# Optimization experiments

Measured on AMD Instinct MI355X. Metric: run time of the kernel, lower is better.

Reference implementation:

```python
import jax, jax.numpy as jnp
import numpy as np

B, C_IN, H, W = 4, 128, 32, 128   # W must equal out_channels (fc_out acts on last dim)
C_OUT, NUM_HEADS = 128, 2
BN_EPS = 1e-5


def setup_inputs() -> dict:
    key = jax.random.key(0)
    ks = jax.random.split(key, 14)
    s = 0.05  # small init scale for weights
    d = {
        "x": jax.random.normal(ks[0], (B, C_IN, H, W), jnp.float32),
        "wq": jax.random.normal(ks[1], (C_OUT, C_IN), jnp.float32) * s,
        "bq": jax.random.normal(ks[2], (C_OUT,), jnp.float32) * s,
        "wk": jax.random.normal(ks[3], (C_OUT, C_IN), jnp.float32) * s,
        "bk": jax.random.normal(ks[4], (C_OUT,), jnp.float32) * s,
        "wv": jax.random.normal(ks[5], (C_OUT, C_IN), jnp.float32) * s,
        "bv": jax.random.normal(ks[6], (C_OUT,), jnp.float32) * s,
        "fc_w": jax.random.normal(ks[7], (C_OUT, C_OUT), jnp.float32) * s,
        "fc_b": jax.random.normal(ks[8], (C_OUT,), jnp.float32) * s,
        "bn_gamma": jnp.ones((C_OUT,), jnp.float32),
        "bn_beta": jnp.zeros((C_OUT,), jnp.float32),
        "bn_mean": jax.random.normal(ks[9], (C_OUT,), jnp.float32) * 0.1,
        "bn_var": jax.random.uniform(ks[10], (C_OUT,), jnp.float32, 0.5, 1.5),
        "prelu_a": jnp.full((1,), 0.25, jnp.float32),
    }
    return d


def reference(x, wq, bq, wk, bk, wv, bv, fc_w, fc_b,
              bn_gamma, bn_beta, bn_mean, bn_var, prelu_a):
    b, c_in, h, w = x.shape
    c_out = wq.shape[0]
    nh = NUM_HEADS
    dk = c_out // nh
    L = h * w
    xf = x.reshape(b, c_in, L)                                # (B, Cin, L)
    # 1x1 convs == per-token linear projections
    q = jnp.einsum('oi,bil->bol', wq, xf) + bq[:, None]       # (B, Cout, L)
    k = jnp.einsum('oi,bil->bol', wk, xf) + bk[:, None]
    v = jnp.einsum('oi,bil->bol', wv, xf) + bv[:, None]
    Q = q.reshape(b, nh, dk, L)                               # (B, h, d_k, L)
    K = k.reshape(b, nh, dk, L)
    V = v.reshape(b, nh, dk, L)
    # scaled dot-product attention over the L = H*W tokens
    scores = jnp.einsum('bhdl,bhdm->bhlm', Q, K) / jnp.sqrt(jnp.float32(dk))
    attn = jax.nn.softmax(scores, axis=-1)                    # (B, h, L, L)
    out = jnp.einsum('bhlm,bhdm->bhdl', attn, V)              # (B, h, d_k, L)
    out = out.reshape(b, c_out, h, w)                         # (B, Cout, H, W)
    # fc_out: torch Linear on the LAST dim (W == Cout)
    y = jnp.einsum('bchw,ow->bcho', out, fc_w) + fc_b         # (B, Cout, H, W)
    # BatchNorm2d (eval mode: running stats) over channel dim
    inv = jax.lax.rsqrt(bn_var + BN_EPS)
    y = (y - bn_mean[None, :, None, None]) * (inv * bn_gamma)[None, :, None, None] \
        + bn_beta[None, :, None, None]
    # PReLU (single shared slope); dropout is identity in eval
    y = jnp.where(y > 0, y, prelu_a[0] * y)
    return y
```

## Files before the change

kernel.cpp:

```cpp
#include <hip/hip_runtime.h>

typedef _Float16 f16x8 __attribute__((ext_vector_type(8)));
typedef _Float16 f16x4t __attribute__((ext_vector_type(4)));
typedef __fp16 h16x2 __attribute__((ext_vector_type(2)));
typedef float f32x4 __attribute__((ext_vector_type(4)));
typedef float f32x16 __attribute__((ext_vector_type(16)));
typedef unsigned int uint2v __attribute__((ext_vector_type(2)));

#define L_SZ 4096

__device__ __forceinline__ unsigned short f2h(float f) {
    _Float16 h = (_Float16)f;
    return __builtin_bit_cast(unsigned short, h);
}
__device__ __forceinline__ unsigned int pk2(float a, float b) {
    h16x2 p = __builtin_amdgcn_cvt_pkrtz(a, b);
    return __builtin_bit_cast(unsigned int, p);
}
__device__ __forceinline__ float fexp2(float x) {
#if __has_builtin(__builtin_amdgcn_exp2f)
    return __builtin_amdgcn_exp2f(x);
#else
    return exp2f(x);
#endif
}
__device__ __forceinline__ float frcp(float x) {
#if __has_builtin(__builtin_amdgcn_rcpf)
    return __builtin_amdgcn_rcpf(x);
#else
    return 1.0f / x;
#endif
}
__device__ __forceinline__ void async16(unsigned short* lds, const unsigned short* g) {
    __builtin_amdgcn_global_load_lds(
        (const __attribute__((address_space(1))) unsigned int*)g,
        (__attribute__((address_space(3))) unsigned int*)lds, 16, 0, 0);
}

#define SLOT(row, ci) ((((ci) * 64) + ((row) & 32) + (((row) & 31) ^ (ci))) * 8)

__global__ __launch_bounds__(256) void prep_kernel(
    const float* __restrict__ wq, const float* __restrict__ wk,
    const float* __restrict__ wv, const float* __restrict__ fcw,
    unsigned short* __restrict__ Wimg, unsigned short* __restrict__ Fimg)
{
    int e2 = blockIdx.x * 256 + threadIdx.x;
    if (e2 < 24576) {
        const float* src = (e2 < 8192) ? wq : (e2 < 16384 ? wk : wv);
        float2 v = *(const float2*)&src[(e2 * 2) & 16383];
        int e = e2 * 2;
        int o = e >> 7, ci = (e & 127) >> 3, j = e & 7;
        *(unsigned int*)&Wimg[o * 128 + ((ci ^ (o & 15)) * 8) + j] = pk2(v.x, v.y);
    } else {
        int fe = (e2 - 24576) * 2;
        float2 v = *(const float2*)&fcw[fe];
        int o = fe >> 7, ci = (fe & 127) >> 3, j = fe & 7;
        *(unsigned int*)&Fimg[o * 128 + ((ci ^ (o & 15)) * 8) + j] = pk2(v.x, v.y);
    }
}

__global__ __launch_bounds__(256, 3) void qkv_kernel(
    const float* __restrict__ x,
    const unsigned short* __restrict__ Wimg,
    const float* __restrict__ bq, const float* __restrict__ bk,
    const float* __restrict__ bv,
    unsigned short* __restrict__ Qp, unsigned short* __restrict__ Kp,
    unsigned short* __restrict__ Vp)
{
    int raw = blockIdx.x;
    int v = (raw & 7) * 96 + (raw >> 3);
    int tile = v / 3;
    int p = v - tile * 3;
    int bidx = tile >> 6;
    int l0 = (tile & 63) * 64;
    int tid = threadIdx.x;
    int wave = tid >> 6, lane = tid & 63;
    int c = lane & 15, qd = lane >> 4;

    __shared__ __align__(16) unsigned short Ws[128 * 128];
    __shared__ __align__(16) unsigned short Sc[9216];

    const unsigned short* wsrc = Wimg + p * 16384;
    #pragma unroll
    for (int t = 0; t < 8; ++t)
        async16(&Ws[(t * 256 + wave * 64) * 8], &wsrc[(size_t)(t * 256 + wave * 64 + lane) * 8]);

    unsigned short* Xs = Sc;
    #pragma unroll
    for (int it = 0; it < 8; ++it) {
        int i  = (tid >> 4) + 16 * it;
        int l4 = (tid & 15) * 4;
        const float4 vx = *(const float4*)&x[(bidx * 128 + i) * L_SZ + l0 + l4];
        float vv[4] = {vx.x, vx.y, vx.z, vx.w};
        int ci = i >> 3;
        #pragma unroll
        for (int u = 0; u < 4; ++u) {
            int l = l4 + u;
            Xs[l * 128 + ((ci ^ (l & 15)) * 8) + (i & 7)] = f2h(vv[u]);
        }
    }
    __syncthreads();

    f16x8 afrag[4];
    #pragma unroll
    for (int kc = 0; kc < 4; ++kc) {
        int l = wave * 16 + c;
        int ci = kc * 4 + qd;
        afrag[kc] = *(const f16x8*)&Xs[l * 128 + ((ci ^ (l & 15)) * 8)];
    }
    __syncthreads();

    f32x4 acc[8];
    #pragma unroll
    for (int nt = 0; nt < 8; ++nt) acc[nt] = (f32x4){0.f, 0.f, 0.f, 0.f};

    #pragma unroll
    for (int kc = 0; kc < 4; ++kc) {
        #pragma unroll
        for (int nt = 0; nt < 8; ++nt) {
            int o = nt * 16 + c;
            f16x8 bfrag = *(const f16x8*)&Ws[o * 128 + (((kc * 4 + qd) ^ c) * 8)];
            acc[nt] = __builtin_amdgcn_mfma_f32_16x16x32_f16(afrag[kc], bfrag, acc[nt], 0, 0, 0);
        }
    }

    const float s_q = 0.18033688011f;
    if (p < 2) {
        const float* bias = (p == 0) ? bq : bk;
        unsigned short* Ot = Sc;
        #pragma unroll
        for (int nt = 0; nt < 8; ++nt) {
            int o = nt * 16 + c;
            float bo = bias[o];
            #pragma unroll
            for (int r = 0; r < 4; ++r) {
                int ll = wave * 16 + qd * 4 + r;
                float val = acc[nt][r] + bo;
                if (p == 0) val *= s_q;
                Ot[ll * 144 + o] = f2h(val);
            }
        }
        __syncthreads();
        unsigned short* dst = (p == 0) ? Qp : Kp;
        #pragma unroll
        for (int t = 0; t < 4; ++t) {
            int u = tid + t * 256;
            int row = u >> 4, col = (u & 15) * 8;
            int h = col >> 6, d = col & 63;
            uint4 a = *(const uint4*)&Ot[row * 144 + col];
            *(uint4*)&dst[((size_t)(bidx * 2 + h) * L_SZ + l0 + row) * 64 + d] = a;
        }
    } else {
        unsigned short* Vt = Sc;
        #pragma unroll
        for (int nt = 0; nt < 8; ++nt) {
            int o = nt * 16 + c;
            #pragma unroll
            for (int r = 0; r < 4; ++r) {
                int ll = wave * 16 + qd * 4 + r;
                Vt[o * 72 + ll] = f2h(acc[nt][r] + bv[o]);
            }
        }
        __syncthreads();
        #pragma unroll
        for (int t = 0; t < 2; ++t) {
            int u = tid + t * 256;
            int row = u >> 2;
            int lc = (u & 3) * 16;
            uint4 a0 = *(const uint4*)&Vt[row * 72 + lc];
            uint4 a1 = *(const uint4*)&Vt[row * 72 + lc + 8];
            *(uint4*)&Vp[(size_t)(bidx * 128 + row) * L_SZ + l0 + lc] = a0;
            *(uint4*)&Vp[(size_t)(bidx * 128 + row) * L_SZ + l0 + lc + 8] = a1;
        }
    }
}

__global__ __launch_bounds__(256, 4) void attn_kernel(
    const unsigned short* __restrict__ Qp, const unsigned short* __restrict__ Kp,
    const unsigned short* __restrict__ Vp,
    unsigned short* __restrict__ Opart, float* __restrict__ Mpart, float* __restrict__ Lpart)
{
    int raw = blockIdx.x;
    int blk = (raw & 7) * 128 + (raw >> 3);
    int lt = blk & 31;
    int bh = (blk >> 5) & 7;
    int sp = blk >> 8;
    int l0 = lt * 128;
    int tid = threadIdx.x;
    int wave = tid >> 6, lane = tid & 63;
    int ln = lane & 31, hi = lane >> 5;
    int b = bh >> 1, h = bh & 1;

    __shared__ __align__(16) unsigned short Ks[2][4096];
    __shared__ __align__(16) unsigned short Vs[2][4096];

    const unsigned short* Qb = Qp + (size_t)bh * L_SZ * 64;
    const unsigned short* Kb = Kp + (size_t)bh * L_SZ * 64;
    const unsigned short* Vb = Vp + ((size_t)b * 128 + h * 64) * L_SZ;

    int lq = l0 + wave * 32 + ln;
    f16x8 qf[4];
    #pragma unroll
    for (int kc = 0; kc < 4; ++kc)
        qf[kc] = *(const f16x8*)&Qb[(size_t)lq * 64 + kc * 16 + hi * 8];

    float m_st = 0.f, lsum = 0.f;
    f32x16 acc0 = {}, acc1 = {};

    int mglob = sp * 1024;
    int ci0 = wave, ci1 = 4 + wave;
    int r0_ = (lane & 32) | ((lane & 31) ^ ci0);
    int r1_ = (lane & 32) | ((lane & 31) ^ ci1);

#define STAGE(t, buf) do {                                                        \
        int m0_ = mglob + (t) * 64;                                               \
        async16(&Ks[buf][(wave * 64) * 8],       &Kb[(size_t)(m0_ + r0_) * 64 + ci0 * 8]); \
        async16(&Ks[buf][(256 + wave * 64) * 8], &Kb[(size_t)(m0_ + r1_) * 64 + ci1 * 8]); \
        async16(&Vs[buf][(wave * 64) * 8],       &Vb[(size_t)r0_ * L_SZ + m0_ + ci0 * 8]); \
        async16(&Vs[buf][(256 + wave * 64) * 8], &Vb[(size_t)r1_ * L_SZ + m0_ + ci1 * 8]); \
    } while (0)

#define QK_COMPUTE(kb) do {                                                       \
        s0 = (f32x16){}; s1 = (f32x16){};                                         \
        _Pragma("unroll")                                                         \
        for (int kc = 0; kc < 4; ++kc) {                                          \
            int cd = kc * 2 + hi;                                                 \
            f16x8 k0 = *(const f16x8*)&Ks[kb][SLOT(ln, cd)];                      \
            f16x8 k1 = *(const f16x8*)&Ks[kb][SLOT(32 + ln, cd)];                 \
            s0 = __builtin_amdgcn_mfma_f32_32x32x16_f16(k0, qf[kc], s0, 0, 0, 0); \
            s1 = __builtin_amdgcn_mfma_f32_32x32x16_f16(k1, qf[kc], s1, 0, 0, 0); \
        }                                                                         \
    } while (0)

#define SM_PV_GROUP(kc, vb, e0,e1,e2,e3,e4,e5,e6,e7, rs) do {                     \
        float p0 = fexp2((e0) - m_st); float p1 = fexp2((e1) - m_st);             \
        float p2 = fexp2((e2) - m_st); float p3 = fexp2((e3) - m_st);             \
        float p4 = fexp2((e4) - m_st); float p5 = fexp2((e5) - m_st);             \
        float p6 = fexp2((e6) - m_st); float p7 = fexp2((e7) - m_st);             \
        rs += ((p0 + p1) + (p2 + p3)) + ((p4 + p5) + (p6 + p7));                  \
        unsigned int a0 = pk2(p0, p1), a1 = pk2(p2, p3);                          \
        unsigned int a2 = pk2(p4, p5), a3 = pk2(p6, p7);                          \
        uint2v r02 = __builtin_amdgcn_permlane32_swap(a0, a2, false, false);      \
        uint2v r13 = __builtin_amdgcn_permlane32_swap(a1, a3, false, false);      \
        uint4 pw; pw.x = r02[0]; pw.y = r13[0]; pw.z = r02[1]; pw.w = r13[1];     \
        f16x8 pf = __builtin_bit_cast(f16x8, pw);                                 \
        int cd = (kc) * 2 + hi;                                                   \
        f16x8 v0 = *(const f16x8*)&Vs[vb][SLOT(ln, cd)];                          \
        f16x8 v1 = *(const f16x8*)&Vs[vb][SLOT(32 + ln, cd)];                     \
        acc0 = __builtin_amdgcn_mfma_f32_32x32x16_f16(v0, pf, acc0, 0, 0, 0);     \
        acc1 = __builtin_amdgcn_mfma_f32_32x32x16_f16(v1, pf, acc1, 0, 0, 0);     \
    } while (0)

#define SM_PV_ALL(vb, rsA, rsB) do {                                              \
        SM_PV_GROUP(0, vb, s0[0],s0[1],s0[2],s0[3],s0[4],s0[5],s0[6],s0[7], rsA); \
        SM_PV_GROUP(1, vb, s0[8],s0[9],s0[10],s0[11],s0[12],s0[13],s0[14],s0[15], rsB); \
        SM_PV_GROUP(2, vb, s1[0],s1[1],s1[2],s1[3],s1[4],s1[5],s1[6],s1[7], rsA); \
        SM_PV_GROUP(3, vb, s1[8],s1[9],s1[10],s1[11],s1[12],s1[13],s1[14],s1[15], rsB); \
    } while (0)

    f32x16 s0, s1;

    STAGE(0, 0);
    __syncthreads();
    STAGE(1, 1);
    __builtin_amdgcn_s_setprio(1);
    QK_COMPUTE(0);
    {
        float t_[8];
        #pragma unroll
        for (int r = 0; r < 8; ++r)
            t_[r] = fmaxf(fmaxf(s0[r], s0[r + 8]), s1[r]);
        #pragma unroll
        for (int r = 0; r < 4; ++r)
            t_[r] = fmaxf(fmaxf(t_[r], t_[r + 4]), s1[8 + r]);
        float m01 = fmaxf(fmaxf(t_[0], t_[1]), s1[12]);
        float m23 = fmaxf(fmaxf(t_[2], t_[3]), s1[13]);
        float mx = fmaxf(fmaxf(m01, m23), fmaxf(s1[14], s1[15]));
        m_st = fmaxf(mx, __shfl_xor(mx, 32));
    }
    {
        float rsA = 0.f, rsB = 0.f;
        SM_PV_ALL(0, rsA, rsB);
        lsum = rsA + rsB;
    }
    __builtin_amdgcn_s_setprio(0);

    for (int t = 1; t < 16; ++t) {
        int cur = t & 1;
        __syncthreads();
        if (t < 15) STAGE(t + 1, cur ^ 1);

        __builtin_amdgcn_s_setprio(1);
        QK_COMPUTE(cur);
        float rsA = 0.f, rsB = 0.f;
        SM_PV_ALL(cur, rsA, rsB);
        lsum += rsA + rsB;
        __builtin_amdgcn_s_setprio(0);
    }
#undef STAGE
#undef QK_COMPUTE
#undef SM_PV_GROUP
#undef SM_PV_ALL

    float l_tot = lsum + __shfl_xor(lsum, 32);
    unsigned short* Ow = Opart + (size_t)(sp * 8 + bh) * 64 * 4096;
    #pragma unroll
    for (int r = 0; r < 16; ++r) {
        int d0 = (r & 3) + 8 * (r >> 2) + 4 * hi;
        Ow[(size_t)d0 * 4096 + lq] = f2h(acc0[r]);
        Ow[(size_t)(32 + d0) * 4096 + lq] = f2h(acc1[r]);
    }
    if (hi == 0) {
        Mpart[(sp * 8 + bh) * 4096 + lq] = m_st;
        Lpart[(sp * 8 + bh) * 4096 + lq] = l_tot;
    }
}

__global__ __launch_bounds__(256) void scl_kernel(
    const float* __restrict__ Mp, const float* __restrict__ Lp,
    unsigned short* __restrict__ SclImg)
{
    int gid = blockIdx.x * 256 + threadIdx.x;
    int bh = gid >> 12, l = gid & 4095;
    float m0 = Mp[(0 * 8 + bh) * 4096 + l], m1 = Mp[(1 * 8 + bh) * 4096 + l];
    float m2 = Mp[(2 * 8 + bh) * 4096 + l], m3 = Mp[(3 * 8 + bh) * 4096 + l];
    float mx = fmaxf(fmaxf(m0, m1), fmaxf(m2, m3));
    float a0 = fexp2(m0 - mx), a1 = fexp2(m1 - mx);
    float a2 = fexp2(m2 - mx), a3 = fexp2(m3 - mx);
    float den = a0 * Lp[(0 * 8 + bh) * 4096 + l] + a1 * Lp[(1 * 8 + bh) * 4096 + l]
              + a2 * Lp[(2 * 8 + bh) * 4096 + l] + a3 * Lp[(3 * 8 + bh) * 4096 + l];
    float inv = frcp(den);
    int hl = l >> 7, ww = l & 127;
    int slot = hl * 128 + ((ww + hl) & 127);
    uint2 sc;
    sc.x = pk2(a0 * inv, a1 * inv);
    sc.y = pk2(a2 * inv, a3 * inv);
    *(uint2*)&SclImg[((size_t)bh * 4096 + slot) * 4] = sc;
}

__global__ __launch_bounds__(256, 2) void fc_kernel(
    const unsigned short* __restrict__ Opart,
    const unsigned short* __restrict__ SclImg,
    const unsigned short* __restrict__ Fimg,
    const float* __restrict__ fc_b, const float* __restrict__ bn_g,
    const float* __restrict__ bn_b, const float* __restrict__ bn_m,
    const float* __restrict__ bn_v, const float* __restrict__ prelu_a,
    float* __restrict__ out)
{
    int raw = blockIdx.x;
    int blk = (raw & 7) * 64 + (raw >> 3);
    int r0 = blk * 32;
    int tid = threadIdx.x;
    int c0 = blk & 127;
    int bh = blk >> 6;
    int d = c0 & 63;

    int wave = tid >> 6, lane = tid & 63;
    int c = lane & 15, qd = lane >> 4;
    int rw = r0 + (wave >> 1) * 16;
    int o0 = (wave & 1) * 64;
    int hh = (rw + c) & 31;

    __shared__ __align__(16) unsigned short Fw[128 * 128];
    __shared__ __align__(16) unsigned short SclU[4096 * 4];

    #pragma unroll
    for (int t = 0; t < 8; ++t)
        async16(&SclU[(t * 256 + wave * 64) * 8],
                &SclImg[(size_t)bh * 16384 + (size_t)(t * 256 + wave * 64 + lane) * 8]);
    #pragma unroll
    for (int t = 0; t < 8; ++t)
        async16(&Fw[(t * 256 + wave * 64) * 8],
                &Fimg[(size_t)(t * 256 + wave * 64 + lane) * 8]);

    uint4 ovr[4][4];
    #pragma unroll
    for (int kc = 0; kc < 4; ++kc) {
        int w0 = kc * 32 + qd * 8;
        #pragma unroll
        for (int s = 0; s < 4; ++s)
            ovr[kc][s] = *(const uint4*)&Opart[(size_t)(s * 8 + bh) * 262144 + (size_t)d * 4096 + hh * 128 + w0];
    }
    __syncthreads();

    f16x8 af[4];
    #pragma unroll
    for (int kc = 0; kc < 4; ++kc) {
        int w0 = kc * 32 + qd * 8;
        f16x8 ov0 = __builtin_bit_cast(f16x8, ovr[kc][0]);
        f16x8 ov1 = __builtin_bit_cast(f16x8, ovr[kc][1]);
        f16x8 ov2 = __builtin_bit_cast(f16x8, ovr[kc][2]);
        f16x8 ov3 = __builtin_bit_cast(f16x8, ovr[kc][3]);
        #pragma unroll
        for (int j = 0; j < 8; ++j) {
            int slot = hh * 128 + ((w0 + j + hh) & 127);
            f16x4t sc = *(const f16x4t*)&SclU[slot * 4];
            float v = (float)ov0[j] * (float)sc[0] + (float)ov1[j] * (float)sc[1]
                    + (float)ov2[j] * (float)sc[2] + (float)ov3[j] * (float)sc[3];
            af[kc][j] = (_Float16)v;
        }
    }

    f32x4 acc[4];
    #pragma unroll
    for (int nt = 0; nt < 4; ++nt) acc[nt] = (f32x4){0.f, 0.f, 0.f, 0.f};
    #pragma unroll
    for (int kc = 0; kc < 4; ++kc) {
        #pragma unroll
        for (int nt = 0; nt < 4; ++nt) {
            int o = o0 + nt * 16 + c;
            f16x8 bf = *(const f16x8*)&Fw[o * 128 + (((kc * 4 + qd) ^ c) * 8)];
            acc[nt] = __builtin_amdgcn_mfma_f32_16x16x32_f16(af[kc], bf, acc[nt], 0, 0, 0);
        }
    }

    float pa = prelu_a[0];
    float g  = bn_g[c0] * rsqrtf(bn_v[c0] + 1e-5f);
    float mn = bn_m[c0], bt = bn_b[c0];
    #pragma unroll
    for (int r = 0; r < 4; ++r) {
        int orow = rw + qd * 4 + r;
        #pragma unroll
        for (int nt = 0; nt < 4; ++nt) {
            int o = o0 + nt * 16 + c;
            float y = (acc[nt][r] + fc_b[o] - mn) * g + bt;
            y = y > 0.f ? y : pa * y;
            out[(size_t)orow * 128 + o] = y;
        }
    }
}

extern "C" void kernel_launch(void* const* d_in, const int* in_sizes, int n_in,
                              void* d_out, int out_size, void* d_ws, size_t ws_size,
                              hipStream_t stream) {
    const float* x     = (const float*)d_in[0];
    const float* wq    = (const float*)d_in[1];
    const float* bq    = (const float*)d_in[2];
    const float* wk    = (const float*)d_in[3];
    const float* bk    = (const float*)d_in[4];
    const float* wv    = (const float*)d_in[5];
    const float* bv    = (const float*)d_in[6];
    const float* fcw_f = (const float*)d_in[7];
    const float* fcb   = (const float*)d_in[8];
    const float* bn_g  = (const float*)d_in[9];
    const float* bn_b  = (const float*)d_in[10];
    const float* bn_m  = (const float*)d_in[11];
    const float* bn_v  = (const float*)d_in[12];
    const float* pa    = (const float*)d_in[13];
    float* out = (float*)d_out;

    unsigned short* Qp  = (unsigned short*)d_ws;
    unsigned short* Kp  = Qp + 8 * L_SZ * 64;
    unsigned short* Vp  = Kp + 8 * L_SZ * 64;
    unsigned short* Opart = Vp + 8 * L_SZ * 64;
    float* Mpart = (float*)(Opart + 4 * 8 * 64 * L_SZ);
    float* Lpart = Mpart + 4 * 8 * L_SZ;
    unsigned short* Wimg   = (unsigned short*)(Lpart + 4 * 8 * L_SZ);
    unsigned short* Fimg   = Wimg + 384 * 128;
    unsigned short* SclImg = Fimg + 128 * 128;

    hipLaunchKernelGGL(prep_kernel, dim3(128),  dim3(256), 0, stream,
                       wq, wk, wv, fcw_f, Wimg, Fimg);
    hipLaunchKernelGGL(qkv_kernel,  dim3(768),  dim3(256), 0, stream,
                       x, Wimg, bq, bk, bv, Qp, Kp, Vp);
    hipLaunchKernelGGL(attn_kernel, dim3(1024), dim3(256), 0, stream,
                       Qp, Kp, Vp, Opart, Mpart, Lpart);
    hipLaunchKernelGGL(scl_kernel,  dim3(128),  dim3(256), 0, stream,
                       Mpart, Lpart, SclImg);
    hipLaunchKernelGGL(fc_kernel,   dim3(512),  dim3(256), 0, stream,
                       Opart, SclImg, Fimg, fcb, bn_g, bn_b, bn_m, bn_v, pa, out);
}
```

Before: 157.7 us.

## Double attention block size to 512 threads with 128-key stages

```diff
diff --git a/kernel.cpp b/kernel.cpp
--- a/kernel.cpp
+++ b/kernel.cpp
@@ -175,24 +175,24 @@
     }
 }
 
-__global__ __launch_bounds__(256, 4) void attn_kernel(
+__global__ __launch_bounds__(512, 4) void attn_kernel(
     const unsigned short* __restrict__ Qp, const unsigned short* __restrict__ Kp,
     const unsigned short* __restrict__ Vp,
     unsigned short* __restrict__ Opart, float* __restrict__ Mpart, float* __restrict__ Lpart)
 {
     int raw = blockIdx.x;
-    int blk = (raw & 7) * 128 + (raw >> 3);
-    int lt = blk & 31;
-    int bh = (blk >> 5) & 7;
-    int sp = blk >> 8;
-    int l0 = lt * 128;
+    int blk = (raw & 7) * 64 + (raw >> 3);
+    int lt = blk & 15;
+    int bh = (blk >> 4) & 7;
+    int sp = blk >> 7;
+    int l0 = lt * 256;
     int tid = threadIdx.x;
     int wave = tid >> 6, lane = tid & 63;
     int ln = lane & 31, hi = lane >> 5;
     int b = bh >> 1, h = bh & 1;
 
-    __shared__ __align__(16) unsigned short Ks[2][4096];
-    __shared__ __align__(16) unsigned short Vs[2][4096];
+    __shared__ __align__(16) unsigned short Ks[2][8192];
+    __shared__ __align__(16) unsigned short Vs[2][8192];
 
     const unsigned short* Qb = Qp + (size_t)bh * L_SZ * 64;
     const unsigned short* Kb = Kp + (size_t)bh * L_SZ * 64;
@@ -208,31 +208,35 @@
     f32x16 acc0 = {}, acc1 = {};
 
     int mglob = sp * 1024;
-    int ci0 = wave, ci1 = 4 + wave;
+    int wv = wave & 3, sh = wave >> 2;
+    int ci0 = wv, ci1 = 4 + wv;
     int r0_ = (lane & 32) | ((lane & 31) ^ ci0);
     int r1_ = (lane & 32) | ((lane & 31) ^ ci1);
 
 #define STAGE(t, buf) do {                                                        \
-        int m0_ = mglob + (t) * 64;                                               \
-        async16(&Ks[buf][(wave * 64) * 8],       &Kb[(size_t)(m0_ + r0_) * 64 + ci0 * 8]); \
-        async16(&Ks[buf][(256 + wave * 64) * 8], &Kb[(size_t)(m0_ + r1_) * 64 + ci1 * 8]); \
-        async16(&Vs[buf][(wave * 64) * 8],       &Vb[(size_t)r0_ * L_SZ + m0_ + ci0 * 8]); \
-        async16(&Vs[buf][(256 + wave * 64) * 8], &Vb[(size_t)r1_ * L_SZ + m0_ + ci1 * 8]); \
+        int m0_ = mglob + (t) * 128 + sh * 64;                                    \
+        unsigned short* kb_ = &Ks[buf][sh * 4096];                                \
+        unsigned short* vb_ = &Vs[buf][sh * 4096];                                \
+        async16(&kb_[(wv * 64) * 8],       &Kb[(size_t)(m0_ + r0_) * 64 + ci0 * 8]); \
+        async16(&kb_[(256 + wv * 64) * 8], &Kb[(size_t)(m0_ + r1_) * 64 + ci1 * 8]); \
+        async16(&vb_[(wv * 64) * 8],       &Vb[(size_t)r0_ * L_SZ + m0_ + ci0 * 8]); \
+        async16(&vb_[(256 + wv * 64) * 8], &Vb[(size_t)r1_ * L_SZ + m0_ + ci1 * 8]); \
     } while (0)
 
-#define QK_COMPUTE(kb) do {                                                       \
+#define QK_COMPUTE(kb, hf) do {                                                   \
+        const unsigned short* Khf = &Ks[kb][(hf) * 4096];                         \
         s0 = (f32x16){}; s1 = (f32x16){};                                         \
         _Pragma("unroll")                                                         \
         for (int kc = 0; kc < 4; ++kc) {                                          \
             int cd = kc * 2 + hi;                                                 \
-            f16x8 k0 = *(const f16x8*)&Ks[kb][SLOT(ln, cd)];                      \
-            f16x8 k1 = *(const f16x8*)&Ks[kb][SLOT(32 + ln, cd)];                 \
+            f16x8 k0 = *(const f16x8*)&Khf[SLOT(ln, cd)];                         \
+            f16x8 k1 = *(const f16x8*)&Khf[SLOT(32 + ln, cd)];                    \
             s0 = __builtin_amdgcn_mfma_f32_32x32x16_f16(k0, qf[kc], s0, 0, 0, 0); \
             s1 = __builtin_amdgcn_mfma_f32_32x32x16_f16(k1, qf[kc], s1, 0, 0, 0); \
         }                                                                         \
     } while (0)
 
-#define SM_PV_GROUP(kc, vb, e0,e1,e2,e3,e4,e5,e6,e7, rs) do {                     \
+#define SM_PV_GROUP(kc, Vhf, e0,e1,e2,e3,e4,e5,e6,e7, rs) do {                    \
         float p0 = fexp2((e0) - m_st); float p1 = fexp2((e1) - m_st);             \
         float p2 = fexp2((e2) - m_st); float p3 = fexp2((e3) - m_st);             \
         float p4 = fexp2((e4) - m_st); float p5 = fexp2((e5) - m_st);             \
@@ -245,17 +249,20 @@
         uint4 pw; pw.x = r02[0]; pw.y = r13[0]; pw.z = r02[1]; pw.w = r13[1];     \
         f16x8 pf = __builtin_bit_cast(f16x8, pw);                                 \
         int cd = (kc) * 2 + hi;                                                   \
-        f16x8 v0 = *(const f16x8*)&Vs[vb][SLOT(ln, cd)];                          \
-        f16x8 v1 = *(const f16x8*)&Vs[vb][SLOT(32 + ln, cd)];                     \
+        f16x8 v0 = *(const f16x8*)&Vhf[SLOT(ln, cd)];                             \
+        f16x8 v1 = *(const f16x8*)&Vhf[SLOT(32 + ln, cd)];                        \
         acc0 = __builtin_amdgcn_mfma_f32_32x32x16_f16(v0, pf, acc0, 0, 0, 0);     \
         acc1 = __builtin_amdgcn_mfma_f32_32x32x16_f16(v1, pf, acc1, 0, 0, 0);     \
     } while (0)
 
-#define SM_PV_ALL(vb, rsA, rsB) do {                                              \
-        SM_PV_GROUP(0, vb, s0[0],s0[1],s0[2],s0[3],s0[4],s0[5],s0[6],s0[7], rsA); \
-        SM_PV_GROUP(1, vb, s0[8],s0[9],s0[10],s0[11],s0[12],s0[13],s0[14],s0[15], rsB); \
-        SM_PV_GROUP(2, vb, s1[0],s1[1],s1[2],s1[3],s1[4],s1[5],s1[6],s1[7], rsA); \
-        SM_PV_GROUP(3, vb, s1[8],s1[9],s1[10],s1[11],s1[12],s1[13],s1[14],s1[15], rsB); \
+#define SM_PV_ALL(vb, hf) do {                                                    \
+        const unsigned short* Vhf = &Vs[vb][(hf) * 4096];                         \
+        float rsA = 0.f, rsB = 0.f;                                               \
+        SM_PV_GROUP(0, Vhf, s0[0],s0[1],s0[2],s0[3],s0[4],s0[5],s0[6],s0[7], rsA); \
+        SM_PV_GROUP(1, Vhf, s0[8],s0[9],s0[10],s0[11],s0[12],s0[13],s0[14],s0[15], rsB); \
+        SM_PV_GROUP(2, Vhf, s1[0],s1[1],s1[2],s1[3],s1[4],s1[5],s1[6],s1[7], rsA); \
+        SM_PV_GROUP(3, Vhf, s1[8],s1[9],s1[10],s1[11],s1[12],s1[13],s1[14],s1[15], rsB); \
+        lsum += rsA + rsB;                                                        \
     } while (0)
 
     f32x16 s0, s1;
@@ -264,7 +271,7 @@
     __syncthreads();
     STAGE(1, 1);
     __builtin_amdgcn_s_setprio(1);
-    QK_COMPUTE(0);
+    QK_COMPUTE(0, 0);
     {
         float t_[8];
         #pragma unroll
@@ -278,23 +285,21 @@
         float mx = fmaxf(fmaxf(m01, m23), fmaxf(s1[14], s1[15]));
         m_st = fmaxf(mx, __shfl_xor(mx, 32));
     }
-    {
-        float rsA = 0.f, rsB = 0.f;
-        SM_PV_ALL(0, rsA, rsB);
-        lsum = rsA + rsB;
-    }
+    SM_PV_ALL(0, 0);
+    QK_COMPUTE(0, 1);
+    SM_PV_ALL(0, 1);
     __builtin_amdgcn_s_setprio(0);
 
-    for (int t = 1; t < 16; ++t) {
+    for (int t = 1; t < 8; ++t) {
         int cur = t & 1;
         __syncthreads();
-        if (t < 15) STAGE(t + 1, cur ^ 1);
+        if (t < 7) STAGE(t + 1, cur ^ 1);
 
         __builtin_amdgcn_s_setprio(1);
-        QK_COMPUTE(cur);
-        float rsA = 0.f, rsB = 0.f;
-        SM_PV_ALL(cur, rsA, rsB);
-        lsum += rsA + rsB;
+        QK_COMPUTE(cur, 0);
+        SM_PV_ALL(cur, 0);
+        QK_COMPUTE(cur, 1);
+        SM_PV_ALL(cur, 1);
         __builtin_amdgcn_s_setprio(0);
     }
 #undef STAGE
@@ -463,7 +468,7 @@
                        wq, wk, wv, fcw_f, Wimg, Fimg);
     hipLaunchKernelGGL(qkv_kernel,  dim3(768),  dim3(256), 0, stream,
                        x, Wimg, bq, bk, bv, Qp, Kp, Vp);
-    hipLaunchKernelGGL(attn_kernel, dim3(1024), dim3(256), 0, stream,
+    hipLaunchKernelGGL(attn_kernel, dim3(512),  dim3(512), 0, stream,
                        Qp, Kp, Vp, Opart, Mpart, Lpart);
     hipLaunchKernelGGL(scl_kernel,  dim3(128),  dim3(256), 0, stream,
                        Mpart, Lpart, SclImg);
```

Result: slower. 173.1 us (+9.7%).
